# Optimization experiments

Hardware: AMD Instinct MI355X
Metric: run time of the kernel (lower is better)

## Reference

```python
import jax, jax.numpy as jnp
import numpy as np

# ---- static configuration (mirrors init_kwargs) ----
B, V, C, NH, HD = 1, 6, 256, 8, 32     # batch, views, embed, heads, head_dim
Z, L, P = 4, 4, 2                       # z-ref points, fmap levels, ref points
BEV_H, BEV_W = 80, 80
Q = BEV_H * BEV_W
IMG_H, IMG_W = 480, 800
LEVEL_SHAPES = [(60, 100), (30, 50), (15, 25), (8, 13)]
S = sum(h * w for h, w in LEVEL_SHAPES)
RES = 0.512
OFFSET_SCALE = 1.0
FF = 512


def layer_norm(x, g, b):
    m = jnp.mean(x, -1, keepdims=True)
    v = jnp.var(x, -1, keepdims=True)
    return (x - m) / jnp.sqrt(v + 1e-5) * g + b


def _bev_grid():
    xs = (jnp.arange(BEV_W) + 0.5) / BEV_W
    ys = (jnp.arange(BEV_H) + 0.5) / BEV_H
    gy, gx = jnp.meshgrid(ys, xs, indexing='ij')
    ref = jnp.stack([gx.reshape(-1), gy.reshape(-1)], -1)        # (Q,2) normalized xy
    world = (ref - 0.5) * jnp.array([BEV_W * RES, BEV_H * RES])  # (Q,2) ego-frame meters
    return ref, world


def deform_sample(value, H, W, loc):
    """Bilinear sampling. value: (N, H*W, NH, HD); loc: (N, Qn, NH, PP, 2) in [0,1].
    Returns (N, Qn, NH, PP, HD); out-of-bounds samples contribute zero."""
    v = jnp.moveaxis(value, 2, 1)                                # (N, NH, HW, HD)
    x = loc[..., 0] * W - 0.5
    y = loc[..., 1] * H - 0.5
    x0 = jnp.floor(x); y0 = jnp.floor(y)
    lx, ly = x - x0, y - y0
    x0 = x0.astype(jnp.int32); y0 = y0.astype(jnp.int32)
    gather = jax.vmap(jax.vmap(lambda vt, it: vt[it]))           # over (N, NH)
    def corner(xi, yi, w):
        ok = ((xi >= 0) & (xi < W) & (yi >= 0) & (yi < H)).astype(value.dtype)
        idx = jnp.clip(yi, 0, H - 1) * W + jnp.clip(xi, 0, W - 1)
        g = gather(v, jnp.moveaxis(idx, 2, 1))                   # (N,NH,Qn,PP,HD)
        return jnp.moveaxis(g, 1, 2) * (w * ok)[..., None]
    return (corner(x0, y0, (1 - lx) * (1 - ly)) + corner(x0 + 1, y0, lx * (1 - ly))
            + corner(x0, y0 + 1, (1 - lx) * ly) + corner(x0 + 1, y0 + 1, lx * ly))


def _forward(bev_queries, bev_histories, multiscale_fmaps, transition_matrices, z_refs,
             cam_proj_matrices, Wv_t, Woff_t, boff_t, Ww_t, bw_t, Wo_t, bo_t, ln1_g, ln1_b,
             Wv_s, Woff_s, boff_s, Ww_s, bw_s, Wo_s, bo_s, ln2_g, ln2_b,
             W1, b1, W2, b2, ln3_g, ln3_b):
    ref, world = _bev_grid()
    q = bev_queries
    # ---------- temporal self-attention (deformable over current + warped history) ----------
    vcur = (q @ Wv_t).reshape(B, Q, NH, HD)
    vhist = (bev_histories @ Wv_t).reshape(B, Q, NH, HD)
    off_t = (q @ Woff_t + boff_t).reshape(B, Q, NH, 2, P, 2) * OFFSET_SCALE
    w_t = jax.nn.softmax((q @ Ww_t + bw_t).reshape(B, Q, NH, 2 * P), -1).reshape(B, Q, NH, 2, P)
    ext = jnp.array([BEV_W * RES, BEV_H * RES], jnp.float32)
    wh = jnp.concatenate([world, jnp.ones((Q, 1), jnp.float32)], -1)     # (Q,3)
    warped = jnp.einsum('bij,qj->bqi', transition_matrices, wh)          # (B,Q,3)
    ref_hist = warped[..., :2] / warped[..., 2:3] / ext + 0.5            # (B,Q,2)
    norm_bev = jnp.array([BEV_W, BEV_H], jnp.float32)
    loc_c = ref[None, :, None, None, :] + off_t[:, :, :, 0] / norm_bev
    loc_h = ref_hist[:, :, None, None, :] + off_t[:, :, :, 1] / norm_bev
    s_c = deform_sample(vcur, BEV_H, BEV_W, loc_c)                       # (B,Q,NH,P,HD)
    s_h = deform_sample(vhist, BEV_H, BEV_W, loc_h)
    out_t = (jnp.einsum('bqhp,bqhpd->bqhd', w_t[:, :, :, 0], s_c)
             + jnp.einsum('bqhp,bqhpd->bqhd', w_t[:, :, :, 1], s_h))
    out1 = out_t.reshape(B, Q, C) @ Wo_t + bo_t
    out2 = layer_norm(out1 + q, ln1_g, ln1_b)
    # ---------- spatial cross-attention (multi-view multi-scale deformable) ----------
    val = (multiscale_fmaps @ Wv_s).reshape(B * V, S, NH, HD)
    pts = jnp.concatenate([
        jnp.broadcast_to(world[:, None, :], (Q, Z, 2)),
        jnp.broadcast_to(z_refs[None, :, None], (Q, Z, 1)),
        jnp.ones((Q, Z, 1), jnp.float32)], -1)                           # (Q,Z,4) homogeneous
    uvd = jnp.einsum('vij,qzj->vqzi', cam_proj_matrices, pts)            # (V,Q,Z,3)
    d = uvd[..., 2]
    un = uvd[..., 0] / jnp.maximum(d, 1e-5) / IMG_W
    vn = uvd[..., 1] / jnp.maximum(d, 1e-5) / IMG_H
    valid = ((d > 1e-5) & (un >= 0) & (un <= 1) & (vn >= 0) & (vn <= 1)).astype(q.dtype)
    refuv = jnp.stack([un, vn], -1)                                      # (V,Q,Z,2)
    off_s = (out2 @ Woff_s + boff_s).reshape(B, Q, NH, Z, L, P, 2) * OFFSET_SCALE
    w_s = jax.nn.softmax((out2 @ Ww_s + bw_s).reshape(B, Q, NH, Z * L * P), -1)
    w_s = w_s.reshape(B, Q, NH, Z, L, P)
    acc = jnp.zeros((B, Q, NH, HD), q.dtype)
    start = 0
    for l, (Hl, Wl) in enumerate(LEVEL_SHAPES):
        vl = val[:, start:start + Hl * Wl]
        start += Hl * Wl
        loc = (refuv[None, :, :, None, :, None, :]
               + off_s[:, None, :, :, :, l] / jnp.array([Wl, Hl], jnp.float32))
        loc = jnp.broadcast_to(loc, (B, V, Q, NH, Z, P, 2)).reshape(B * V, Q, NH, Z * P, 2)
        samp = deform_sample(vl, Hl, Wl, loc).reshape(B, V, Q, NH, Z, P, HD)
        wl = w_s[:, None, :, :, :, l] * valid[None, :, :, None, :, None]
        acc = acc + jnp.einsum('bvqhzp,bvqhzpd->bqhd', wl, samp)
    count = jnp.maximum(valid.sum((0, 2)), 1.0)                          # (Q,) hit count
    out3 = (acc / count[None, :, None, None]).reshape(B, Q, C) @ Wo_s + bo_s
    out4 = layer_norm(out3 + out2, ln2_g, ln2_b)
    # ---------- feed-forward ----------
    out5 = jax.nn.relu(out4 @ W1 + b1) @ W2 + b2
    return layer_norm(out5 + out4, ln3_g, ln3_b)


def setup_inputs() -> dict:
    key = jax.random.key(0)
    ks = iter(jax.random.split(key, 40))
    def rn(shape, s=1.0):
        return jax.random.normal(next(ks), shape, jnp.float32) * s
    sc = 1.0 / float(np.sqrt(C))
    inp = {}
    inp['bev_queries'] = rn((B, Q, C), 0.1)
    inp['bev_histories'] = rn((B, Q, C), 0.1)
    inp['multiscale_fmaps'] = rn((B, V, S, C), 0.1)
    th = 0.02
    T = np.array([[np.cos(th), -np.sin(th), 0.5],
                  [np.sin(th), np.cos(th), 0.1],
                  [0.0, 0.0, 1.0]], np.float32)
    inp['transition_matrices'] = jnp.tile(jnp.asarray(T)[None], (B, 1, 1))
    inp['z_refs'] = jnp.linspace(-5.0, 3.0, Z).astype(jnp.float32)
    K = np.array([[400.0, 0.0, IMG_W / 2], [0.0, 400.0, IMG_H / 2], [0.0, 0.0, 1.0]], np.float32)
    Ps = []
    for vi in range(V):
        a = 2 * np.pi * vi / V
        Rt = np.zeros((3, 4), np.float32)
        Rt[0, :3] = [-np.sin(a), np.cos(a), 0.0]   # camera right
        Rt[1, :3] = [0.0, 0.0, -1.0]               # camera down
        Rt[2, :3] = [np.cos(a), np.sin(a), 0.0]    # camera forward
        Ps.append(K @ Rt)
    inp['cam_proj_matrices'] = jnp.asarray(np.stack(Ps))
    # temporal self-attention params
    inp['Wv_t'] = rn((C, C), sc)
    inp['Woff_t'] = rn((C, NH * 2 * P * 2), sc * 0.1)
    inp['boff_t'] = jnp.zeros((NH * 2 * P * 2,), jnp.float32)
    inp['Ww_t'] = rn((C, NH * 2 * P), sc)
    inp['bw_t'] = jnp.zeros((NH * 2 * P,), jnp.float32)
    inp['Wo_t'] = rn((C, C), sc)
    inp['bo_t'] = jnp.zeros((C,), jnp.float32)
    inp['ln1_g'] = jnp.ones((C,), jnp.float32)
    inp['ln1_b'] = jnp.zeros((C,), jnp.float32)
    # spatial cross-attention params
    inp['Wv_s'] = rn((C, C), sc)
    inp['Woff_s'] = rn((C, NH * Z * L * P * 2), sc * 0.1)
    inp['boff_s'] = jnp.zeros((NH * Z * L * P * 2,), jnp.float32)
    inp['Ww_s'] = rn((C, NH * Z * L * P), sc)
    inp['bw_s'] = jnp.zeros((NH * Z * L * P,), jnp.float32)
    inp['Wo_s'] = rn((C, C), sc)
    inp['bo_s'] = jnp.zeros((C,), jnp.float32)
    inp['ln2_g'] = jnp.ones((C,), jnp.float32)
    inp['ln2_b'] = jnp.zeros((C,), jnp.float32)
    # FFN params
    inp['W1'] = rn((C, FF), sc)
    inp['b1'] = jnp.zeros((FF,), jnp.float32)
    inp['W2'] = rn((FF, C), 1.0 / float(np.sqrt(FF)))
    inp['b2'] = jnp.zeros((C,), jnp.float32)
    inp['ln3_g'] = jnp.ones((C,), jnp.float32)
    inp['ln3_b'] = jnp.zeros((C,), jnp.float32)
    # static shape descriptors (treated as compile-time constants)
    inp['bev_spatial_shape'] = np.array([[BEV_H, BEV_W]], np.int64)
    inp['multiscale_fmap_shapes'] = np.array(LEVEL_SHAPES, np.int64)
    inp['img_spatial_shape'] = np.array([[IMG_H, IMG_W]], np.int64)
    return inp


def reference(bev_queries, bev_histories, multiscale_fmaps, transition_matrices, z_refs,
              cam_proj_matrices, Wv_t, Woff_t, boff_t, Ww_t, bw_t, Wo_t, bo_t, ln1_g, ln1_b,
              Wv_s, Woff_s, boff_s, Ww_s, bw_s, Wo_s, bo_s, ln2_g, ln2_b,
              W1, b1, W2, b2, ln3_g, ln3_b,
              bev_spatial_shape, multiscale_fmap_shapes, img_spatial_shape):
    return _forward(bev_queries, bev_histories, multiscale_fmaps, transition_matrices, z_refs,
                    cam_proj_matrices, Wv_t, Woff_t, boff_t, Ww_t, bw_t, Wo_t, bo_t, ln1_g, ln1_b,
                    Wv_s, Woff_s, boff_s, Ww_s, bw_s, Wo_s, bo_s, ln2_g, ln2_b,
                    W1, b1, W2, b2, ln3_g, ln3_b)
```

## Files before the change

kernel.cpp:

```cpp
#include <hip/hip_runtime.h>
#include <hip/hip_bf16.h>
#include <hip/hip_fp16.h>

typedef unsigned short u16;
typedef unsigned int u32;
typedef __attribute__((ext_vector_type(8))) _Float16 f16x8;
typedef __attribute__((ext_vector_type(4))) float f32x4;

#define Q_N  6400
#define S_N  7979
#define BEV  80

__device__ __forceinline__ float f16tof(u16 u) {
    __half h; *(u16*)&h = u; return __half2float(h);
}
__device__ __forceinline__ u16 ftof16(float f) {
    __half h = __float2half(f); return *(u16*)&h;
}

template <int AIN, int RELU, int OUTMODE, int SM4, int SM32>
__device__ __forceinline__ void gemm_body(
    const void* __restrict__ A, const u16* __restrict__ WT,
    const float* __restrict__ bias, const float* __restrict__ bias2,
    void* __restrict__ Cout, int M, int N, int K, int bx, int by,
    u16* Ah, u16* Wh)
{
    const int tid  = threadIdx.x;
    const int lane = tid & 63;
    const int wave = tid >> 6;
    const int wm = (wave >> 1) * 32, wn = (wave & 1) * 64;
    const int m0 = by * 64, n0 = bx * 128;
    const int arow = tid >> 2, ak = (tid & 3) * 8;
    const int wrow = tid >> 1, wk = (tid & 1) * 16;
    const int fr = lane & 15, g = lane >> 4;

    f32x4 acc[8];
    #pragma unroll
    for (int i = 0; i < 8; ++i) acc[i] = (f32x4)(0.f);

    for (int k0 = 0; k0 < K; k0 += 32) {
        {
            const bool okr = (m0 + arow) < M;
            u16* dh = &Ah[arow * 40 + ak];
            if (AIN == 0) {
                const float* ap = (const float*)A + (size_t)(m0 + arow) * K + k0 + ak;
                float4 v0 = okr ? *(const float4*)(ap)     : make_float4(0.f, 0.f, 0.f, 0.f);
                float4 v1 = okr ? *(const float4*)(ap + 4) : make_float4(0.f, 0.f, 0.f, 0.f);
                u16 hb[8];
                hb[0] = ftof16(v0.x); hb[1] = ftof16(v0.y);
                hb[2] = ftof16(v0.z); hb[3] = ftof16(v0.w);
                hb[4] = ftof16(v1.x); hb[5] = ftof16(v1.y);
                hb[6] = ftof16(v1.z); hb[7] = ftof16(v1.w);
                *(ushort4*)(dh)     = *(ushort4*)&hb[0];
                *(ushort4*)(dh + 4) = *(ushort4*)&hb[4];
            } else {
                const u16* ap = (const u16*)A + (size_t)(m0 + arow) * K + k0 + ak;
                uint4 u = okr ? *(const uint4*)ap : make_uint4(0, 0, 0, 0);
                *(uint4*)dh = u;
            }
        }
        {
            const size_t wo = (size_t)(n0 + wrow) * K + k0 + wk;
            *(uint4*)&Wh[wrow * 40 + wk]     = *(const uint4*)(WT + wo);
            *(uint4*)&Wh[wrow * 40 + wk + 8] = *(const uint4*)(WT + wo + 8);
        }
        __syncthreads();
        f16x8 fah[2], fwh[4];
        #pragma unroll
        for (int i = 0; i < 2; ++i)
            fah[i] = *(const f16x8*)&Ah[(wm + i * 16 + fr) * 40 + g * 8];
        #pragma unroll
        for (int j = 0; j < 4; ++j)
            fwh[j] = *(const f16x8*)&Wh[(wn + j * 16 + fr) * 40 + g * 8];
        #pragma unroll
        for (int i = 0; i < 2; ++i)
            #pragma unroll
            for (int j = 0; j < 4; ++j)
                acc[i * 4 + j] = __builtin_amdgcn_mfma_f32_16x16x32_f16(fah[i], fwh[j], acc[i * 4 + j], 0, 0, 0);
        __syncthreads();
    }
    const int g4r = g * 4;
    float bv[4];
    #pragma unroll
    for (int j = 0; j < 4; ++j) {
        int col = n0 + wn + j * 16 + fr;
        if (bias2) bv[j] = (col < 512) ? bias[col] : bias2[col - 512];
        else       bv[j] = bias ? bias[col] : 0.f;
    }
    const bool do_sm4  = SM4 && (wn == 64);
    #pragma unroll
    for (int i = 0; i < 2; ++i) {
        #pragma unroll
        for (int r = 0; r < 4; ++r) {
            const int row = m0 + wm + i * 16 + g4r + r;
            float v0 = acc[i * 4 + 0][r] + bv[0];
            float v1 = acc[i * 4 + 1][r] + bv[1];
            float v2 = acc[i * 4 + 2][r] + bv[2];
            float v3 = acc[i * 4 + 3][r] + bv[3];
            if (RELU) {
                v0 = fmaxf(v0, 0.f); v1 = fmaxf(v1, 0.f);
                v2 = fmaxf(v2, 0.f); v3 = fmaxf(v3, 0.f);
            }
            if (SM4 && do_sm4) {
                float m0q = fmaxf(v0, __shfl_xor(v0, 1));
                m0q = fmaxf(m0q, __shfl_xor(m0q, 2));
                float e0 = __expf(v0 - m0q);
                float s0 = e0 + __shfl_xor(e0, 1);
                s0 += __shfl_xor(s0, 2);
                v0 = e0 / s0;
                float m1q = fmaxf(v1, __shfl_xor(v1, 1));
                m1q = fmaxf(m1q, __shfl_xor(m1q, 2));
                float e1 = __expf(v1 - m1q);
                float s1 = e1 + __shfl_xor(e1, 1);
                s1 += __shfl_xor(s1, 2);
                v1 = e1 / s1;
                v2 = 0.f; v3 = 0.f;
            }
            if (row < M) {
                const int colb = n0 + wn + fr;
                if (OUTMODE == 1) {
                    u16* cp = (u16*)Cout + (size_t)row * N;
                    cp[colb]      = ftof16(v0);
                    cp[colb + 16] = ftof16(v1);
                    cp[colb + 32] = ftof16(v2);
                    cp[colb + 48] = ftof16(v3);
                } else {
                    float* cp = (float*)Cout + (size_t)row * N;
                    cp[colb]      = v0;
                    cp[colb + 16] = v1;
                    cp[colb + 32] = v2;
                    cp[colb + 48] = v3;
                }
            }
        }
    }
}

__global__ __launch_bounds__(256) void fused3_k(
    const float* __restrict__ fmaps, const float* __restrict__ q, const float* __restrict__ hist,
    const u16* __restrict__ Wv_s_h, const u16* __restrict__ Wv_t_h,
    const u16* __restrict__ Wc_h, const float* __restrict__ bc,
    u16* __restrict__ val_f16, u16* __restrict__ vcur, u16* __restrict__ vhist,
    float* __restrict__ owt)
{
    __shared__ u16 Ah[64 * 40], Wh[128 * 40];
    const int b = blockIdx.x;
    if (b < 1498) {
        gemm_body<0, 0, 1, 0, 0>(fmaps, Wv_s_h, nullptr, nullptr, val_f16,
                                 47874, 256, 256, b & 1, b >> 1, Ah, Wh);
    } else if (b < 1698) {
        int l = b - 1498;
        gemm_body<0, 0, 1, 0, 0>(q, Wv_t_h, nullptr, nullptr, vcur,
                                 6400, 256, 256, l & 1, l >> 1, Ah, Wh);
    } else if (b < 1898) {
        int l = b - 1698;
        gemm_body<0, 0, 1, 0, 0>(hist, Wv_t_h, nullptr, nullptr, vhist,
                                 6400, 256, 256, l & 1, l >> 1, Ah, Wh);
    } else {
        int l = b - 1898;
        gemm_body<0, 0, 0, 1, 0>(q, Wc_h, bc, nullptr, owt,
                                 6400, 128, 256, 0, l, Ah, Wh);
    }
}

template <int AIN, int RELU, int OUTMODE, int SM4, int SM32>
__global__ __launch_bounds__(256, 2) void sgemm_k(
    const void* __restrict__ A, const u16* __restrict__ WT,
    const float* __restrict__ bias, const float* __restrict__ bias2,
    void* __restrict__ Cout, int M, int N, int K)
{
    __shared__ u16 Ah[8][1288];
    __shared__ u16 Wh[8][2568];
    const int tid  = threadIdx.x;
    const int lane = tid & 63;
    const int wave = tid >> 6;
    const int wm = (wave >> 1) * 16, wn = (wave & 1) * 32;
    const int m0 = blockIdx.y * 32, n0 = blockIdx.x * 64;
    const int fr = lane & 15, g = lane >> 4;

    const int ar  = tid >> 3, cch = tid & 7;
    const int wrow = tid >> 2, wc4 = tid & 3;

    f32x4 acc[2] = {(f32x4)(0.f), (f32x4)(0.f)};

    for (int k0 = 0; k0 < K; k0 += 256) {
        if (k0) __syncthreads();
        {
            const bool okr = (m0 + ar) < M;
            u16 hb[32];
            if (AIN == 0) {
                const float* ap = (const float*)A + (size_t)(m0 + ar) * K + k0 + cch * 32;
                #pragma unroll
                for (int i = 0; i < 8; ++i) {
                    float4 v = okr ? *(const float4*)(ap + i * 4) : make_float4(0.f, 0.f, 0.f, 0.f);
                    hb[i * 4 + 0] = ftof16(v.x); hb[i * 4 + 1] = ftof16(v.y);
                    hb[i * 4 + 2] = ftof16(v.z); hb[i * 4 + 3] = ftof16(v.w);
                }
            } else {
                const u16* ap = (const u16*)A + (size_t)(m0 + ar) * K + k0 + cch * 32;
                #pragma unroll
                for (int i = 0; i < 4; ++i)
                    *(uint4*)&hb[i * 8] = okr ? *(const uint4*)(ap + i * 8) : make_uint4(0, 0, 0, 0);
            }
            u16* dst = &Ah[cch][ar * 40];
            #pragma unroll
            for (int i = 0; i < 8; ++i)
                *(ushort4*)(dst + i * 4) = *(ushort4*)&hb[i * 4];
        }
        {
            const size_t wo = (size_t)(n0 + wrow) * K + k0 + wc4 * 64;
            #pragma unroll
            for (int half = 0; half < 2; ++half) {
                u16* dst = &Wh[wc4 * 2 + half][wrow * 40];
                const u16* src = WT + wo + half * 32;
                #pragma unroll
                for (int i = 0; i < 4; ++i)
                    *(uint4*)(dst + i * 8) = *(const uint4*)(src + i * 8);
            }
        }
        __syncthreads();
        #pragma unroll
        for (int c = 0; c < 8; ++c) {
            f16x8 fa  = *(const f16x8*)&Ah[c][(wm + fr) * 40 + g * 8];
            f16x8 fw0 = *(const f16x8*)&Wh[c][(wn + fr) * 40 + g * 8];
            f16x8 fw1 = *(const f16x8*)&Wh[c][(wn + 16 + fr) * 40 + g * 8];
            acc[0] = __builtin_amdgcn_mfma_f32_16x16x32_f16(fa, fw0, acc[0], 0, 0, 0);
            acc[1] = __builtin_amdgcn_mfma_f32_16x16x32_f16(fa, fw1, acc[1], 0, 0, 0);
        }
    }
    const int g4r = g * 4;
    const int c0g = n0 + wn + fr, c1g = c0g + 16;
    float bv0, bv1;
    if (bias2) {
        bv0 = (c0g < 512) ? bias[c0g] : bias2[c0g - 512];
        bv1 = (c1g < 512) ? bias[c1g] : bias2[c1g - 512];
    } else {
        bv0 = bias ? bias[c0g] : 0.f;
        bv1 = bias ? bias[c1g] : 0.f;
    }
    const bool do_sm32 = SM32 && ((n0 + wn) >= 512);
    const bool do_sm4  = SM4 && ((n0 + wn) == 64);
    const bool zr4     = SM4 && ((n0 + wn) == 96);
    #pragma unroll
    for (int r = 0; r < 4; ++r) {
        const int row = m0 + wm + g4r + r;
        float v0 = acc[0][r] + bv0;
        float v1 = acc[1][r] + bv1;
        if (RELU) { v0 = fmaxf(v0, 0.f); v1 = fmaxf(v1, 0.f); }
        if (SM4) {
            if (do_sm4) {
                float m0q = fmaxf(v0, __shfl_xor(v0, 1));
                m0q = fmaxf(m0q, __shfl_xor(m0q, 2));
                float e0 = __expf(v0 - m0q);
                float s0 = e0 + __shfl_xor(e0, 1);
                s0 += __shfl_xor(s0, 2);
                v0 = e0 / s0;
                float m1q = fmaxf(v1, __shfl_xor(v1, 1));
                m1q = fmaxf(m1q, __shfl_xor(m1q, 2));
                float e1 = __expf(v1 - m1q);
                float s1 = e1 + __shfl_xor(e1, 1);
                s1 += __shfl_xor(s1, 2);
                v1 = e1 / s1;
            }
            if (zr4) { v0 = 0.f; v1 = 0.f; }
        }
        if (SM32 && do_sm32) {
            float ma = fmaxf(v0, v1);
            ma = fmaxf(ma, __shfl_xor(ma, 1));
            ma = fmaxf(ma, __shfl_xor(ma, 2));
            ma = fmaxf(ma, __shfl_xor(ma, 4));
            ma = fmaxf(ma, __shfl_xor(ma, 8));
            float e0 = __expf(v0 - ma), e1 = __expf(v1 - ma);
            float sa = e0 + e1;
            sa += __shfl_xor(sa, 1);
            sa += __shfl_xor(sa, 2);
            sa += __shfl_xor(sa, 4);
            sa += __shfl_xor(sa, 8);
            float ia = 1.f / sa;
            v0 = e0 * ia; v1 = e1 * ia;
        }
        if (row < M) {
            if (OUTMODE == 1) {
                u16* cp = (u16*)Cout + (size_t)row * N;
                cp[c0g] = ftof16(v0);
                cp[c1g] = ftof16(v1);
            } else {
                float* cp = (float*)Cout + (size_t)row * N;
                cp[c0g] = v0;
                cp[c1g] = v1;
            }
        }
    }
}

__global__ __launch_bounds__(256) void wprep_k(
    const float* __restrict__ w0, const float* __restrict__ w1, const float* __restrict__ w2,
    const float* __restrict__ w3, const float* __restrict__ w4, const float* __restrict__ w5,
    const float* __restrict__ w6, const float* __restrict__ w7, u16* __restrict__ base,
    const float* __restrict__ Woff_t, const float* __restrict__ Ww_t,
    const float* __restrict__ boff_t, const float* __restrict__ bw_t,
    float* __restrict__ bc)
{
    const int b = blockIdx.x, tid = threadIdx.x;
    if (b == 184) {
        if (tid < 128) bc[tid] = (tid < 64) ? boff_t[tid] : (tid < 96 ? bw_t[tid - 64] : 0.f);
        return;
    }
    const int cum[10]  = {0, 16, 32, 48, 80, 96, 112, 144, 176, 184};
    const int Ks[9]    = {256, 256, 256, 256, 256, 256, 256, 512, 256};
    const int Ns[9]    = {256, 256, 256, 512, 256, 256, 512, 256, 128};
    const int hoff[9]  = {0, 65536, 131072, 196608, 327680, 393216, 458752, 589824, 720896};
    int seg = 0;
    #pragma unroll
    for (int s = 1; s < 9; ++s) if (b >= cum[s]) seg = s;
    const int K = Ks[seg], N = Ns[seg];
    const int t = b - cum[seg];
    const int ntn = N / 64;
    const int k0 = (t / ntn) * 64, n0 = (t % ntn) * 64;
    __shared__ float tile[64][65];
    const int rr = tid >> 2, cc = (tid & 3) * 16;
    if (seg < 8) {
        const float* W = seg == 0 ? w0 : seg == 1 ? w1 : seg == 2 ? w2 : seg == 3 ? w3 :
                         seg == 4 ? w4 : seg == 5 ? w5 : seg == 6 ? w6 : w7;
        #pragma unroll
        for (int c = 0; c < 4; ++c) {
            float4 v = *(const float4*)(W + (size_t)(k0 + rr) * N + n0 + cc + c * 4);
            tile[rr][cc + c * 4 + 0] = v.x;
            tile[rr][cc + c * 4 + 1] = v.y;
            tile[rr][cc + c * 4 + 2] = v.z;
            tile[rr][cc + c * 4 + 3] = v.w;
        }
    } else {
        #pragma unroll
        for (int i = 0; i < 16; ++i) {
            int n = n0 + cc + i, k = k0 + rr;
            float v = (n < 64) ? Woff_t[k * 64 + n] : (n < 96 ? Ww_t[k * 32 + n - 64] : 0.f);
            tile[rr][cc + i] = v;
        }
    }
    __syncthreads();
    const int nr = tid >> 2, kc = (tid & 3) * 16;
    u16 hb[16];
    #pragma unroll
    for (int i = 0; i < 16; ++i) hb[i] = ftof16(tile[kc + i][nr]);
    u16* hp = base + hoff[seg] + (size_t)(n0 + nr) * K + k0 + kc;
    *(ushort4*)(hp + 0)  = *(ushort4*)&hb[0];
    *(ushort4*)(hp + 4)  = *(ushort4*)&hb[4];
    *(ushort4*)(hp + 8)  = *(ushort4*)&hb[8];
    *(ushort4*)(hp + 12) = *(ushort4*)&hb[12];
}

__global__ __launch_bounds__(256) void ln_k(
    const float* __restrict__ x, const float* __restrict__ res,
    const float* __restrict__ g, const float* __restrict__ b,
    float* __restrict__ out)
{
    const int row = blockIdx.x, t = threadIdx.x;
    const size_t idx = (size_t)row * 256 + t;
    float v = x[idx] + res[idx];
    float s = v, ss = v * v;
    #pragma unroll
    for (int o = 32; o > 0; o >>= 1) {
        s += __shfl_down(s, o);
        ss += __shfl_down(ss, o);
    }
    __shared__ float red[8];
    __shared__ float mv[2];
    const int wv = t >> 6, ln = t & 63;
    if (ln == 0) { red[wv] = s; red[4 + wv] = ss; }
    __syncthreads();
    if (t == 0) {
        float S = red[0] + red[1] + red[2] + red[3];
        float SS = red[4] + red[5] + red[6] + red[7];
        float mean = S * (1.f / 256.f);
        float var = SS * (1.f / 256.f) - mean * mean;
        mv[0] = mean;
        mv[1] = rsqrtf(var + 1e-5f);
    }
    __syncthreads();
    out[idx] = (v - mv[0]) * mv[1] * g[t] + b[t];
}

__device__ __forceinline__ float4 bilin4h(const u16* __restrict__ v, int H, int W,
                                          float x, float y, int chb)
{
    float xf = floorf(x), yf = floorf(y);
    int x0 = (int)xf, y0 = (int)yf;
    int x1 = x0 + 1, y1 = y0 + 1;
    float fx = x - xf, fy = y - yf;
    float w00 = (1.f - fx) * (1.f - fy), w10 = fx * (1.f - fy);
    float w01 = (1.f - fx) * fy,         w11 = fx * fy;
    bool xi0 = (x0 >= 0) && (x0 < W);
    bool xi1 = (x1 >= 0) && (x1 < W);
    bool yi0 = (y0 >= 0) && (y0 < H);
    bool yi1 = (y1 >= 0) && (y1 < H);
    float4 r = make_float4(0.f, 0.f, 0.f, 0.f);
    #define CORNER(xi, yi, xx, yy, ww)                                           \
        if ((yi) && (xi)) {                                                      \
            uint2 u = *(const uint2*)(v + ((size_t)(yy) * W + (xx)) * 256 + chb);\
            float2 f0 = __half22float2(*(const __half2*)&u.x);                   \
            float2 f1 = __half22float2(*(const __half2*)&u.y);                   \
            r.x += (ww) * f0.x; r.y += (ww) * f0.y;                              \
            r.z += (ww) * f1.x; r.w += (ww) * f1.y;                              \
        }
    CORNER(xi0, yi0, x0, y0, w00)
    CORNER(xi1, yi0, x1, y0, w10)
    CORNER(xi0, yi1, x0, y1, w01)
    CORNER(xi1, yi1, x1, y1, w11)
    #undef CORNER
    return r;
}

__global__ __launch_bounds__(256) void temporal_k(
    const u16* __restrict__ vcur, const u16* __restrict__ vhist,
    const float* __restrict__ ow,
    const float* __restrict__ Tm, float* __restrict__ outt)
{
    const int b = blockIdx.x;
    const int q = (b & 7) * 800 + (b >> 3);
    const int tid = threadIdx.x;
    const int c4 = tid & 63, rep = tid >> 6;
    const int br = rep >> 1, p = rep & 1;
    const int h = c4 >> 3;
    const int chb = h * 32 + (c4 & 7) * 4;
    const int jx = q % BEV, iy = q / BEV;
    const float refx = (jx + 0.5f) / 80.f;
    const float refy = (iy + 0.5f) / 80.f;
    const float wx = (refx - 0.5f) * 40.96f;
    const float wy = (refy - 0.5f) * 40.96f;
    float bx, by;
    const u16* v;
    if (br == 0) { v = vcur; bx = refx; by = refy; }
    else {
        float h0 = Tm[0] * wx + Tm[1] * wy + Tm[2];
        float h1 = Tm[3] * wx + Tm[4] * wy + Tm[5];
        float h2 = Tm[6] * wx + Tm[7] * wy + Tm[8];
        v = vhist;
        bx = h0 / h2 / 40.96f + 0.5f;
        by = h1 / h2 / 40.96f + 0.5f;
    }
    const float* owq = ow + (size_t)q * 128;
    int ob = h * 8 + br * 4 + p * 2;
// ... 50 lines not shown
        const u16* owq = ow + (size_t)q * 768;
        #pragma unroll
        for (int rep = 0; rep < 2; ++rep) {
            int flat = tid + rep * 256;
            int hh = flat >> 6, rem = flat & 63;
            int zz = rem >> 4, ll = (rem >> 2) & 3, pp = (rem >> 1) & 1, xy = rem & 1;
            int dst = (zz * 8 + ll * 2 + pp) * 8 + hh;
            float v = f16tof(owq[flat]);
            if (xy) s_oy[dst] = v; else s_ox[dst] = v;
        }
        int hh = tid >> 5, rem = tid & 31;
        s_wt[rem * 8 + hh] = f16tof(owq[512 + tid]);
    }
    __syncthreads();
    if (tid == 0) {
        int n = 0; float c = 0.f;
        for (int vz = 0; vz < 24; ++vz) {
            if (s_ok[vz] != 0.f) { s_list[n++] = vz; c += 1.f; }
        }
        s_n = n; s_cnt = fmaxf(c, 1.f);
    }
    __syncthreads();
    const int n4 = s_n * 4;
    float a0 = 0.f, a1 = 0.f, a2 = 0.f, a3 = 0.f, a4 = 0.f, a5 = 0.f, a6 = 0.f, a7 = 0.f;
    for (int w = slot; w < n4; w += 8) {
        const int it = w >> 2, l = w & 3;
        const int vz = s_list[it];
        const int v = vz >> 2, z = vz & 3;
        const float un = s_un[vz], vn = s_vn[vz];
        const int Hl  = (l == 0) ? 60  : (l == 1) ? 30   : (l == 2) ? 15   : 8;
        const int Wl  = (l == 0) ? 100 : (l == 1) ? 50   : (l == 2) ? 25   : 13;
        const int LSo = (l == 0) ? 0   : (l == 1) ? 6000 : (l == 2) ? 7500 : 7875;
        const u16* lv = val + ((size_t)v * S_N + LSo) * 256 + chb;
        const float unl = un * Wl - 0.5f, vnl = vn * Hl - 0.5f;
        const int Ws = Wl * 256;
        #pragma unroll
        for (int p = 0; p < 2; ++p) {
            const int idx = (z * 8 + l * 2 + p) * 8 + h;
            float x = unl + s_ox[idx];
            float y = vnl + s_oy[idx];
            float wgt = s_wt[idx];
            float xf = floorf(x), yf = floorf(y);
            int x0 = (int)xf, y0 = (int)yf;
            float fx = x - xf, fy = y - yf;
            bool xi0 = (x0 >= 0) & (x0 < Wl);
            bool xi1 = (x0 >= -1) & (x0 < Wl - 1);
            bool yi0 = (y0 >= 0) & (y0 < Hl);
            bool yi1 = (y0 >= -1) & (y0 < Hl - 1);
            int xc0 = min(max(x0, 0), Wl - 1);
            int xc1 = min(max(x0 + 1, 0), Wl - 1);
            int yc0 = min(max(y0, 0), Hl - 1);
            int yc1 = min(max(y0 + 1, 0), Hl - 1);
            float m00 = (xi0 & yi0) ? wgt : 0.f;
            float m10 = (xi1 & yi0) ? wgt : 0.f;
            float m01 = (xi0 & yi1) ? wgt : 0.f;
            float m11 = (xi1 & yi1) ? wgt : 0.f;
            __half2 w00 = __float2half2_rn((1.f - fx) * (1.f - fy) * m00);
            __half2 w10 = __float2half2_rn(fx * (1.f - fy) * m10);
            __half2 w01 = __float2half2_rn((1.f - fx) * fy * m01);
            __half2 w11 = __float2half2_rn(fx * fy * m11);
            const u16* r0p = lv + (size_t)yc0 * Ws;
            const u16* r1p = lv + (size_t)yc1 * Ws;
            uint4 u00 = *(const uint4*)(r0p + (size_t)xc0 * 256);
            uint4 u10 = *(const uint4*)(r0p + (size_t)xc1 * 256);
            uint4 u01 = *(const uint4*)(r1p + (size_t)xc0 * 256);
            uint4 u11 = *(const uint4*)(r1p + (size_t)xc1 * 256);
            __half2 h0 = __float2half2_rn(0.f), h1 = h0, h2 = h0, h3 = h0;
            {
                const __half2* hp = (const __half2*)&u00;
                h0 = __hfma2(w00, hp[0], h0); h1 = __hfma2(w00, hp[1], h1);
                h2 = __hfma2(w00, hp[2], h2); h3 = __hfma2(w00, hp[3], h3);
            }
            {
                const __half2* hp = (const __half2*)&u10;
                h0 = __hfma2(w10, hp[0], h0); h1 = __hfma2(w10, hp[1], h1);
                h2 = __hfma2(w10, hp[2], h2); h3 = __hfma2(w10, hp[3], h3);
            }
            {
                const __half2* hp = (const __half2*)&u01;
                h0 = __hfma2(w01, hp[0], h0); h1 = __hfma2(w01, hp[1], h1);
                h2 = __hfma2(w01, hp[2], h2); h3 = __hfma2(w01, hp[3], h3);
            }
            {
                const __half2* hp = (const __half2*)&u11;
                h0 = __hfma2(w11, hp[0], h0); h1 = __hfma2(w11, hp[1], h1);
                h2 = __hfma2(w11, hp[2], h2); h3 = __hfma2(w11, hp[3], h3);
            }
            float2 f0 = __half22float2(h0), f1 = __half22float2(h1);
            float2 f2 = __half22float2(h2), f3 = __half22float2(h3);
            a0 += f0.x; a1 += f0.y; a2 += f1.x; a3 += f1.y;
            a4 += f2.x; a5 += f2.y; a6 += f3.x; a7 += f3.y;
        }
    }
    *(float4*)&s_part[slot][chb]     = make_float4(a0, a1, a2, a3);
    *(float4*)&s_part[slot][chb + 4] = make_float4(a4, a5, a6, a7);
    __syncthreads();
    float sum = 0.f;
    #pragma unroll
    for (int k = 0; k < 8; ++k) sum += s_part[k][tid];
    out[(size_t)q * 256 + tid] = sum / s_cnt;
}

extern "C" void kernel_launch(void* const* d_in, const int* in_sizes, int n_in,
                              void* d_out, int out_size, void* d_ws, size_t ws_size,
                              hipStream_t stream) {
    (void)in_sizes; (void)n_in; (void)out_size; (void)ws_size;
    const float* q      = (const float*)d_in[0];
    const float* hist   = (const float*)d_in[1];
    const float* fmaps  = (const float*)d_in[2];
    const float* Tm     = (const float*)d_in[3];
    const float* zrefs  = (const float*)d_in[4];
    const float* cam    = (const float*)d_in[5];
    const float* Woff_t = (const float*)d_in[7];
    const float* boff_t = (const float*)d_in[8];
    const float* Ww_t   = (const float*)d_in[9];
    const float* bw_t   = (const float*)d_in[10];
    const float* bo_t   = (const float*)d_in[12];
    const float* ln1g   = (const float*)d_in[13];
    const float* ln1b   = (const float*)d_in[14];
    const float* boff_s = (const float*)d_in[17];
    const float* bw_s   = (const float*)d_in[19];
    const float* bo_s   = (const float*)d_in[21];
    const float* ln2g   = (const float*)d_in[22];
    const float* ln2b   = (const float*)d_in[23];
    const float* b1     = (const float*)d_in[25];
    const float* b2     = (const float*)d_in[27];
    const float* ln3g   = (const float*)d_in[28];
    const float* ln3b   = (const float*)d_in[29];

    float* ws    = (float*)d_ws;
    float* r0    = ws;
    float* r1    = ws + 1638400;
    float* owt   = ws + 3276800;
    float* r4    = ws + 4096000;
    u16*  r5u    = (u16*)(ws + 5734400);
    float* of4   = ws + 8192000;
    u16*  valbuf = (u16*)(ws + 9830400);
    u16*  vcur   = (u16*)(ws + 15958272);
    u16*  vhist  = (u16*)(ws + 16777472);
    u16*  wtab   = (u16*)(ws + 17596672);
    float* bc    = ws + 18350336;

    u16* hidden = valbuf;
    u16* Wv_t_h = wtab + 0;
    u16* Wo_t_h = wtab + 65536;
    u16* Wv_s_h = wtab + 131072;
    u16* Comb_h = wtab + 196608;
    u16* Wo_s_h = wtab + 393216;
    u16* W1_h   = wtab + 458752;
    u16* W2_h   = wtab + 589824;
    u16* Wc_h   = wtab + 720896;

    dim3 blk(256);
    auto gs = [](int M, int N) { return dim3((unsigned)(N / 64), (unsigned)((M + 31) / 32)); };

    wprep_k<<<dim3(185), blk, 0, stream>>>(
        (const float*)d_in[6], (const float*)d_in[11], (const float*)d_in[15],
        (const float*)d_in[16], (const float*)d_in[18], (const float*)d_in[20],
        (const float*)d_in[24], (const float*)d_in[26], wtab,
        Woff_t, Ww_t, boff_t, bw_t, bc);
    fused3_k<<<dim3(1998), blk, 0, stream>>>(
        fmaps, q, hist, Wv_s_h, Wv_t_h, Wc_h, bc,
        valbuf, vcur, vhist, owt);
    temporal_k<<<dim3(6400), blk, 0, stream>>>(vcur, vhist, owt, Tm, r4);
    sgemm_k<0,0,0,0,0><<<gs(6400, 256), blk, 0, stream>>>(
        r4, Wo_t_h, bo_t, nullptr, r0, 6400, 256, 256);
    ln_k<<<dim3(6400), blk, 0, stream>>>(r0, q, ln1g, ln1b, r1);
    sgemm_k<0,0,1,0,1><<<gs(6400, 768), blk, 0, stream>>>(
        r1, Comb_h, boff_s, bw_s, r5u, 6400, 768, 256);
    spatial_k<<<dim3(6400), blk, 0, stream>>>(valbuf, r5u, cam, zrefs, r0);
    sgemm_k<0,0,0,0,0><<<gs(6400, 256), blk, 0, stream>>>(
        r0, Wo_s_h, bo_s, nullptr, r4, 6400, 256, 256);
    ln_k<<<dim3(6400), blk, 0, stream>>>(r4, r1, ln2g, ln2b, of4);
    sgemm_k<0,1,1,0,0><<<gs(6400, 512), blk, 0, stream>>>(
        of4, W1_h, b1, nullptr, hidden, 6400, 512, 256);
    sgemm_k<1,0,0,0,0><<<gs(6400, 256), blk, 0, stream>>>(
        hidden, W2_h, b2, nullptr, r0, 6400, 256, 512);
    ln_k<<<dim3(6400), blk, 0, stream>>>(r0, of4, ln3g, ln3b, (float*)d_out);
}
```

Measured before the change: 360.4 us.

## Fuse residual LayerNorm into GEMM A-load and retile GEMMs to 64-row blocks

Replaces the sgemm kernel with a 64x64-tile GEMM that keeps the full 256-wide A strip in shared memory and streams weight K-slices through a double buffer. Two standalone LayerNorm launches are removed: the following GEMM adds the residual, normalizes each row while loading A, and has the blockIdx.x==0 blocks write the normalized rows out for later residual use. This cuts launches and the global round trip for the LN outputs. In exchange every N-block recomputes the LN, and a __syncthreads now runs after each 32-wide K step.

After: 368.1 us. 2.1% more time.

```diff
diff --git a/kernel.cpp b/kernel.cpp
--- a/kernel.cpp
+++ b/kernel.cpp
@@ -163,69 +163,112 @@
     }
 }
 
-template <int AIN, int RELU, int OUTMODE, int SM4, int SM32>
-__global__ __launch_bounds__(256, 2) void sgemm_k(
-    const void* __restrict__ A, const u16* __restrict__ WT,
-    const float* __restrict__ bias, const float* __restrict__ bias2,
+template <int AIN, int RELU, int OUTMODE, int SM32, int LNA>
+__global__ __launch_bounds__(256) void mgemm2_k(
+    const void* __restrict__ A, const float* __restrict__ res,
+    const float* __restrict__ lng, const float* __restrict__ lnb,
+    float* __restrict__ aux,
+    const u16* __restrict__ WT, const float* __restrict__ bias, const float* __restrict__ bias2,
     void* __restrict__ Cout, int M, int N, int K)
 {
-    __shared__ u16 Ah[8][1288];
-    __shared__ u16 Wh[8][2568];
+    __shared__ u16 As[64 * 264];
+    __shared__ u16 Wsh[2][64 * 40];
     const int tid  = threadIdx.x;
     const int lane = tid & 63;
     const int wave = tid >> 6;
-    const int wm = (wave >> 1) * 16, wn = (wave & 1) * 32;
-    const int m0 = blockIdx.y * 32, n0 = blockIdx.x * 64;
+    const int wm = (wave >> 1) * 32, wn = (wave & 1) * 32;
+    const int m0 = blockIdx.y * 64, n0 = blockIdx.x * 64;
     const int fr = lane & 15, g = lane >> 4;
-
-    const int ar  = tid >> 3, cch = tid & 7;
-    const int wrow = tid >> 2, wc4 = tid & 3;
-
-    f32x4 acc[2] = {(f32x4)(0.f), (f32x4)(0.f)};
-
-    for (int k0 = 0; k0 < K; k0 += 256) {
-        if (k0) __syncthreads();
+    const int ar = tid >> 2, aq = tid & 3;
+    const int NSTEP = K >> 5;
+
+    f32x4 acc[4];
+    #pragma unroll
+    for (int i = 0; i < 4; ++i) acc[i] = (f32x4)(0.f);
+
+    for (int kh = 0; kh < K; kh += 256) {
         {
             const bool okr = (m0 + ar) < M;
-            u16 hb[32];
             if (AIN == 0) {
-                const float* ap = (const float*)A + (size_t)(m0 + ar) * K + k0 + cch * 32;
-                #pragma unroll
-                for (int i = 0; i < 8; ++i) {
-                    float4 v = okr ? *(const float4*)(ap + i * 4) : make_float4(0.f, 0.f, 0.f, 0.f);
-                    hb[i * 4 + 0] = ftof16(v.x); hb[i * 4 + 1] = ftof16(v.y);
-                    hb[i * 4 + 2] = ftof16(v.z); hb[i * 4 + 3] = ftof16(v.w);
+                const float* ap = (const float*)A + (size_t)(m0 + ar) * K + kh;
+                if (LNA) {
+                    float4 vals[16];
+                    float s = 0.f, ss = 0.f;
+                    const float* rp = res + (size_t)(m0 + ar) * 256;
+                    #pragma unroll
+                    for (int j = 0; j < 16; ++j) {
+                        const int k = aq * 4 + j * 16;
+                        float4 x = okr ? *(const float4*)(ap + k) : make_float4(0.f, 0.f, 0.f, 0.f);
+                        float4 rr = okr ? *(const float4*)(rp + k) : make_float4(0.f, 0.f, 0.f, 0.f);
+                        x.x += rr.x; x.y += rr.y; x.z += rr.z; x.w += rr.w;
+                        vals[j] = x;
+                        s += x.x + x.y + x.z + x.w;
+                        ss += x.x * x.x + x.y * x.y + x.z * x.z + x.w * x.w;
+                    }
+                    s  += __shfl_xor(s, 1);  s  += __shfl_xor(s, 2);
+                    ss += __shfl_xor(ss, 1); ss += __shfl_xor(ss, 2);
+                    const float mean = s * (1.f / 256.f);
+                    const float rstd = rsqrtf(ss * (1.f / 256.f) - mean * mean + 1e-5f);
+                    const bool wa = (blockIdx.x == 0) && okr;
+                    #pragma unroll
+                    for (int j = 0; j < 16; ++j) {
+                        const int k = aq * 4 + j * 16;
+                        float4 g4 = *(const float4*)(lng + k);
+                        float4 b4 = *(const float4*)(lnb + k);
+                        float4 v = vals[j];
+                        v.x = (v.x - mean) * rstd * g4.x + b4.x;
+                        v.y = (v.y - mean) * rstd * g4.y + b4.y;
+                        v.z = (v.z - mean) * rstd * g4.z + b4.z;
+                        v.w = (v.w - mean) * rstd * g4.w + b4.w;
+                        if (wa) *(float4*)(aux + (size_t)(m0 + ar) * 256 + k) = v;
+                        u16 hb[4];
+                        hb[0] = ftof16(v.x); hb[1] = ftof16(v.y);
+                        hb[2] = ftof16(v.z); hb[3] = ftof16(v.w);
+                        *(ushort4*)&As[ar * 264 + k] = *(ushort4*)&hb[0];
+                    }
+                } else {
+                    #pragma unroll
+                    for (int j = 0; j < 16; ++j) {
+                        const int k = aq * 4 + j * 16;
+                        float4 x = okr ? *(const float4*)(ap + k) : make_float4(0.f, 0.f, 0.f, 0.f);
+                        u16 hb[4];
+                        hb[0] = ftof16(x.x); hb[1] = ftof16(x.y);
+                        hb[2] = ftof16(x.z); hb[3] = ftof16(x.w);
+                        *(ushort4*)&As[ar * 264 + k] = *(ushort4*)&hb[0];
+                    }
                 }
             } else {
-                const u16* ap = (const u16*)A + (size_t)(m0 + ar) * K + k0 + cch * 32;
+                const u16* ap = (const u16*)A + (size_t)(m0 + ar) * K + kh;
                 #pragma unroll
-                for (int i = 0; i < 4; ++i)
-                    *(uint4*)&hb[i * 8] = okr ? *(const uint4*)(ap + i * 8) : make_uint4(0, 0, 0, 0);
-            }
-            u16* dst = &Ah[cch][ar * 40];
-            #pragma unroll
-            for (int i = 0; i < 8; ++i)
-                *(ushort4*)(dst + i * 4) = *(ushort4*)&hb[i * 4];
-        }
-        {
-            const size_t wo = (size_t)(n0 + wrow) * K + k0 + wc4 * 64;
-            #pragma unroll
-            for (int half = 0; half < 2; ++half) {
-                u16* dst = &Wh[wc4 * 2 + half][wrow * 40];
-                const u16* src = WT + wo + half * 32;
-                #pragma unroll
-                for (int i = 0; i < 4; ++i)
-                    *(uint4*)(dst + i * 8) = *(const uint4*)(src + i * 8);
-            }
+                for (int j = 0; j < 8; ++j) {
+                    const int k = aq * 8 + j * 32;
+                    uint4 u = okr ? *(const uint4*)(ap + k) : make_uint4(0, 0, 0, 0);
+                    *(uint4*)&As[ar * 264 + k] = u;
+                }
+            }
+        }
+        if (kh == 0) {
+            *(uint4*)&Wsh[0][ar * 40 + aq * 8] =
+                *(const uint4*)(WT + (size_t)(n0 + ar) * K + aq * 8);
         }
         __syncthreads();
         #pragma unroll
-        for (int c = 0; c < 8; ++c) {
-            f16x8 fa  = *(const f16x8*)&Ah[c][(wm + fr) * 40 + g * 8];
-            f16x8 fw0 = *(const f16x8*)&Wh[c][(wn + fr) * 40 + g * 8];
-            f16x8 fw1 = *(const f16x8*)&Wh[c][(wn + 16 + fr) * 40 + g * 8];
-            acc[0] = __builtin_amdgcn_mfma_f32_16x16x32_f16(fa, fw0, acc[0], 0, 0, 0);
-            acc[1] = __builtin_amdgcn_mfma_f32_16x16x32_f16(fa, fw1, acc[1], 0, 0, 0);
+        for (int s = 0; s < 8; ++s) {
+            const int gstep = (kh >> 5) + s;
+            const int nxt = gstep + 1;
+            if (nxt < NSTEP) {
+                *(uint4*)&Wsh[nxt & 1][ar * 40 + aq * 8] =
+                    *(const uint4*)(WT + (size_t)(n0 + ar) * K + nxt * 32 + aq * 8);
+            }
+            f16x8 fa0 = *(const f16x8*)&As[(wm + fr) * 264 + s * 32 + g * 8];
+            f16x8 fa1 = *(const f16x8*)&As[(wm + 16 + fr) * 264 + s * 32 + g * 8];
+            f16x8 fw0 = *(const f16x8*)&Wsh[s & 1][(wn + fr) * 40 + g * 8];
+            f16x8 fw1 = *(const f16x8*)&Wsh[s & 1][(wn + 16 + fr) * 40 + g * 8];
+            acc[0] = __builtin_amdgcn_mfma_f32_16x16x32_f16(fa0, fw0, acc[0], 0, 0, 0);
+            acc[1] = __builtin_amdgcn_mfma_f32_16x16x32_f16(fa0, fw1, acc[1], 0, 0, 0);
+            acc[2] = __builtin_amdgcn_mfma_f32_16x16x32_f16(fa1, fw0, acc[2], 0, 0, 0);
+            acc[3] = __builtin_amdgcn_mfma_f32_16x16x32_f16(fa1, fw1, acc[3], 0, 0, 0);
+            __syncthreads();
         }
     }
     const int g4r = g * 4;
@@ -239,55 +282,39 @@
         bv1 = bias ? bias[c1g] : 0.f;
     }
     const bool do_sm32 = SM32 && ((n0 + wn) >= 512);
-    const bool do_sm4  = SM4 && ((n0 + wn) == 64);
-    const bool zr4     = SM4 && ((n0 + wn) == 96);
-    #pragma unroll
-    for (int r = 0; r < 4; ++r) {
-        const int row = m0 + wm + g4r + r;
-        float v0 = acc[0][r] + bv0;
-        float v1 = acc[1][r] + bv1;
-        if (RELU) { v0 = fmaxf(v0, 0.f); v1 = fmaxf(v1, 0.f); }
-        if (SM4) {
-            if (do_sm4) {
-                float m0q = fmaxf(v0, __shfl_xor(v0, 1));
-                m0q = fmaxf(m0q, __shfl_xor(m0q, 2));
-                float e0 = __expf(v0 - m0q);
-                float s0 = e0 + __shfl_xor(e0, 1);
-                s0 += __shfl_xor(s0, 2);
-                v0 = e0 / s0;
-                float m1q = fmaxf(v1, __shfl_xor(v1, 1));
-                m1q = fmaxf(m1q, __shfl_xor(m1q, 2));
-                float e1 = __expf(v1 - m1q);
-                float s1 = e1 + __shfl_xor(e1, 1);
-                s1 += __shfl_xor(s1, 2);
-                v1 = e1 / s1;
-            }
-            if (zr4) { v0 = 0.f; v1 = 0.f; }
-        }
-        if (SM32 && do_sm32) {
-            float ma = fmaxf(v0, v1);
-            ma = fmaxf(ma, __shfl_xor(ma, 1));
-            ma = fmaxf(ma, __shfl_xor(ma, 2));
-            ma = fmaxf(ma, __shfl_xor(ma, 4));
-            ma = fmaxf(ma, __shfl_xor(ma, 8));
-            float e0 = __expf(v0 - ma), e1 = __expf(v1 - ma);
-            float sa = e0 + e1;
-            sa += __shfl_xor(sa, 1);
-            sa += __shfl_xor(sa, 2);
-            sa += __shfl_xor(sa, 4);
-            sa += __shfl_xor(sa, 8);
-            float ia = 1.f / sa;
-            v0 = e0 * ia; v1 = e1 * ia;
-        }
-        if (row < M) {
-            if (OUTMODE == 1) {
-                u16* cp = (u16*)Cout + (size_t)row * N;
-                cp[c0g] = ftof16(v0);
-                cp[c1g] = ftof16(v1);
-            } else {
-                float* cp = (float*)Cout + (size_t)row * N;
-                cp[c0g] = v0;
-                cp[c1g] = v1;
+    #pragma unroll
+    for (int i = 0; i < 2; ++i) {
+        #pragma unroll
+        for (int r = 0; r < 4; ++r) {
+            const int row = m0 + wm + i * 16 + g4r + r;
+            float v0 = acc[i * 2 + 0][r] + bv0;
+            float v1 = acc[i * 2 + 1][r] + bv1;
+            if (RELU) { v0 = fmaxf(v0, 0.f); v1 = fmaxf(v1, 0.f); }
+            if (SM32 && do_sm32) {
+                float ma = fmaxf(v0, v1);
+                ma = fmaxf(ma, __shfl_xor(ma, 1));
+                ma = fmaxf(ma, __shfl_xor(ma, 2));
+                ma = fmaxf(ma, __shfl_xor(ma, 4));
+                ma = fmaxf(ma, __shfl_xor(ma, 8));
+                float e0 = __expf(v0 - ma), e1 = __expf(v1 - ma);
+                float sa = e0 + e1;
+                sa += __shfl_xor(sa, 1);
+                sa += __shfl_xor(sa, 2);
+                sa += __shfl_xor(sa, 4);
+                sa += __shfl_xor(sa, 8);
+                float ia = 1.f / sa;
+                v0 = e0 * ia; v1 = e1 * ia;
+            }
+            if (row < M) {
+                if (OUTMODE == 1) {
+                    u16* cp = (u16*)Cout + (size_t)row * N;
+                    cp[c0g] = ftof16(v0);
+                    cp[c1g] = ftof16(v1);
+                } else {
+                    float* cp = (float*)Cout + (size_t)row * N;
+                    cp[c0g] = v0;
+                    cp[c1g] = v1;
+                }
             }
         }
     }
@@ -644,7 +671,7 @@
     u16* Wc_h   = wtab + 720896;
 
     dim3 blk(256);
-    auto gs = [](int M, int N) { return dim3((unsigned)(N / 64), (unsigned)((M + 31) / 32)); };
+    auto g2 = [](int M, int N) { return dim3((unsigned)(N / 64), (unsigned)((M + 63) / 64)); };
 
     wprep_k<<<dim3(185), blk, 0, stream>>>(
         (const float*)d_in[6], (const float*)d_in[11], (const float*)d_in[15],
@@ -655,18 +682,21 @@
         fmaps, q, hist, Wv_s_h, Wv_t_h, Wc_h, bc,
         valbuf, vcur, vhist, owt);
     temporal_k<<<dim3(6400), blk, 0, stream>>>(vcur, vhist, owt, Tm, r4);
-    sgemm_k<0,0,0,0,0><<<gs(6400, 256), blk, 0, stream>>>(
-        r4, Wo_t_h, bo_t, nullptr, r0, 6400, 256, 256);
-    ln_k<<<dim3(6400), blk, 0, stream>>>(r0, q, ln1g, ln1b, r1);
-    sgemm_k<0,0,1,0,1><<<gs(6400, 768), blk, 0, stream>>>(
-        r1, Comb_h, boff_s, bw_s, r5u, 6400, 768, 256);
+    mgemm2_k<0,0,0,0,0><<<g2(6400, 256), blk, 0, stream>>>(
+        r4, nullptr, nullptr, nullptr, nullptr,
+        Wo_t_h, bo_t, nullptr, r0, 6400, 256, 256);
+    mgemm2_k<0,0,1,1,1><<<g2(6400, 768), blk, 0, stream>>>(
+        r0, q, ln1g, ln1b, r1,
+        Comb_h, boff_s, bw_s, r5u, 6400, 768, 256);
     spatial_k<<<dim3(6400), blk, 0, stream>>>(valbuf, r5u, cam, zrefs, r0);
-    sgemm_k<0,0,0,0,0><<<gs(6400, 256), blk, 0, stream>>>(
-        r0, Wo_s_h, bo_s, nullptr, r4, 6400, 256, 256);
-    ln_k<<<dim3(6400), blk, 0, stream>>>(r4, r1, ln2g, ln2b, of4);
-    sgemm_k<0,1,1,0,0><<<gs(6400, 512), blk, 0, stream>>>(
-        of4, W1_h, b1, nullptr, hidden, 6400, 512, 256);
-    sgemm_k<1,0,0,0,0><<<gs(6400, 256), blk, 0, stream>>>(
-        hidden, W2_h, b2, nullptr, r0, 6400, 256, 512);
+    mgemm2_k<0,0,0,0,0><<<g2(6400, 256), blk, 0, stream>>>(
+        r0, nullptr, nullptr, nullptr, nullptr,
+        Wo_s_h, bo_s, nullptr, r4, 6400, 256, 256);
+    mgemm2_k<0,1,1,0,1><<<g2(6400, 512), blk, 0, stream>>>(
+        r4, r1, ln2g, ln2b, of4,
+        W1_h, b1, nullptr, hidden, 6400, 512, 256);
+    mgemm2_k<1,0,0,0,0><<<g2(6400, 256), blk, 0, stream>>>(
+        hidden, nullptr, nullptr, nullptr, nullptr,
+        W2_h, b2, nullptr, r0, 6400, 256, 512);
     ln_k<<<dim3(6400), blk, 0, stream>>>(r0, of4, ln3g, ln3b, (float*)d_out);
 }
```

## Double-buffer GEMM K-loop with register prefetch and swizzled block order

Applied to the files above, without the earlier changes.

Replaces the standalone GEMM kernel's staging of the full 256-wide K slice into large shared memory with a 32-wide K step that is double-buffered. The next slice is prefetched into registers while the MFMAs run on the current one. Shared memory per block drops sharply, launch bounds move to 4 blocks per CU, and workgroup IDs are remapped in groups of 8 to change cache locality. The cost is one barrier per 32-wide K step instead of per 256, plus removal of the row-bound check and the unused SM4 path. That is safe here because M is a multiple of 32.

Result: faster. 304.4 us (-15.6%).

```diff
diff --git a/kernel.cpp b/kernel.cpp
--- a/kernel.cpp
+++ b/kernel.cpp
@@ -163,72 +163,75 @@
     }
 }
 
-template <int AIN, int RELU, int OUTMODE, int SM4, int SM32>
-__global__ __launch_bounds__(256, 2) void sgemm_k(
+template <int AIN, int RELU, int OUTMODE, int SM32>
+__global__ __launch_bounds__(256, 4) void cgemm_k(
     const void* __restrict__ A, const u16* __restrict__ WT,
     const float* __restrict__ bias, const float* __restrict__ bias2,
     void* __restrict__ Cout, int M, int N, int K)
 {
-    __shared__ u16 Ah[8][1288];
-    __shared__ u16 Wh[8][2568];
+    __shared__ u16 As[2][32 * 40];
+    __shared__ u16 Wsh[2][64 * 40];
     const int tid  = threadIdx.x;
     const int lane = tid & 63;
     const int wave = tid >> 6;
     const int wm = (wave >> 1) * 16, wn = (wave & 1) * 32;
-    const int m0 = blockIdx.y * 32, n0 = blockIdx.x * 64;
     const int fr = lane & 15, g = lane >> 4;
-
-    const int ar  = tid >> 3, cch = tid & 7;
-    const int wrow = tid >> 2, wc4 = tid & 3;
+    const int nx = gridDim.x;
+    const int nwg = nx * gridDim.y;
+    const int o = blockIdx.y * nx + blockIdx.x;
+    const int flat = (o & 7) * (nwg >> 3) + (o >> 3);
+    const int bx = flat % nx, by = flat / nx;
+    const int m0 = by * 32, n0 = bx * 64;
+    const int ar = tid >> 3, ak = (tid & 7) * 4;
+    const int wr = tid >> 2, wk = (tid & 3) * 8;
+    const int NS = K >> 5;
 
     f32x4 acc[2] = {(f32x4)(0.f), (f32x4)(0.f)};
 
-    for (int k0 = 0; k0 < K; k0 += 256) {
-        if (k0) __syncthreads();
-        {
-            const bool okr = (m0 + ar) < M;
-            u16 hb[32];
+    const float* apf = (const float*)A + (size_t)(m0 + ar) * K + ak;
+    const u16*  aph  = (const u16*)A + (size_t)(m0 + ar) * K + ak;
+    const u16*  wp   = WT + (size_t)(n0 + wr) * K + wk;
+
+    if (AIN == 0) {
+        float4 v = *(const float4*)apf;
+        u16 hb[4];
+        hb[0] = ftof16(v.x); hb[1] = ftof16(v.y); hb[2] = ftof16(v.z); hb[3] = ftof16(v.w);
+        *(ushort4*)&As[0][ar * 40 + ak] = *(ushort4*)&hb[0];
+    } else {
+        *(uint2*)&As[0][ar * 40 + ak] = *(const uint2*)aph;
+    }
+    *(uint4*)&Wsh[0][wr * 40 + wk] = *(const uint4*)wp;
+    __syncthreads();
+
+    for (int s = 0; s < NS; ++s) {
+        float4 av; uint2 au; uint4 wv;
+        const bool pf = (s + 1) < NS;
+        if (pf) {
+            if (AIN == 0) av = *(const float4*)(apf + (s + 1) * 32);
+            else          au = *(const uint2*)(aph + (s + 1) * 32);
+            wv = *(const uint4*)(wp + (s + 1) * 32);
+        }
+        const int b = s & 1;
+        f16x8 fa  = *(const f16x8*)&As[b][(wm + fr) * 40 + g * 8];
+        f16x8 fw0 = *(const f16x8*)&Wsh[b][(wn + fr) * 40 + g * 8];
+        f16x8 fw1 = *(const f16x8*)&Wsh[b][(wn + 16 + fr) * 40 + g * 8];
+        acc[0] = __builtin_amdgcn_mfma_f32_16x16x32_f16(fa, fw0, acc[0], 0, 0, 0);
+        acc[1] = __builtin_amdgcn_mfma_f32_16x16x32_f16(fa, fw1, acc[1], 0, 0, 0);
+        if (pf) {
+            const int nb = b ^ 1;
             if (AIN == 0) {
-                const float* ap = (const float*)A + (size_t)(m0 + ar) * K + k0 + cch * 32;
-                #pragma unroll
-                for (int i = 0; i < 8; ++i) {
-                    float4 v = okr ? *(const float4*)(ap + i * 4) : make_float4(0.f, 0.f, 0.f, 0.f);
-                    hb[i * 4 + 0] = ftof16(v.x); hb[i * 4 + 1] = ftof16(v.y);
-                    hb[i * 4 + 2] = ftof16(v.z); hb[i * 4 + 3] = ftof16(v.w);
-                }
+                u16 hb[4];
+                hb[0] = ftof16(av.x); hb[1] = ftof16(av.y);
+                hb[2] = ftof16(av.z); hb[3] = ftof16(av.w);
+                *(ushort4*)&As[nb][ar * 40 + ak] = *(ushort4*)&hb[0];
             } else {
-                const u16* ap = (const u16*)A + (size_t)(m0 + ar) * K + k0 + cch * 32;
-                #pragma unroll
-                for (int i = 0; i < 4; ++i)
-                    *(uint4*)&hb[i * 8] = okr ? *(const uint4*)(ap + i * 8) : make_uint4(0, 0, 0, 0);
-            }
-            u16* dst = &Ah[cch][ar * 40];
-            #pragma unroll
-            for (int i = 0; i < 8; ++i)
-                *(ushort4*)(dst + i * 4) = *(ushort4*)&hb[i * 4];
-        }
-        {
-            const size_t wo = (size_t)(n0 + wrow) * K + k0 + wc4 * 64;
-            #pragma unroll
-            for (int half = 0; half < 2; ++half) {
-                u16* dst = &Wh[wc4 * 2 + half][wrow * 40];
-                const u16* src = WT + wo + half * 32;
-                #pragma unroll
-                for (int i = 0; i < 4; ++i)
-                    *(uint4*)(dst + i * 8) = *(const uint4*)(src + i * 8);
-            }
+                *(uint2*)&As[nb][ar * 40 + ak] = au;
+            }
+            *(uint4*)&Wsh[nb][wr * 40 + wk] = wv;
         }
         __syncthreads();
-        #pragma unroll
-        for (int c = 0; c < 8; ++c) {
-            f16x8 fa  = *(const f16x8*)&Ah[c][(wm + fr) * 40 + g * 8];
-            f16x8 fw0 = *(const f16x8*)&Wh[c][(wn + fr) * 40 + g * 8];
-            f16x8 fw1 = *(const f16x8*)&Wh[c][(wn + 16 + fr) * 40 + g * 8];
-            acc[0] = __builtin_amdgcn_mfma_f32_16x16x32_f16(fa, fw0, acc[0], 0, 0, 0);
-            acc[1] = __builtin_amdgcn_mfma_f32_16x16x32_f16(fa, fw1, acc[1], 0, 0, 0);
-        }
-    }
-    const int g4r = g * 4;
+    }
+
     const int c0g = n0 + wn + fr, c1g = c0g + 16;
     float bv0, bv1;
     if (bias2) {
@@ -239,31 +242,12 @@
         bv1 = bias ? bias[c1g] : 0.f;
     }
     const bool do_sm32 = SM32 && ((n0 + wn) >= 512);
-    const bool do_sm4  = SM4 && ((n0 + wn) == 64);
-    const bool zr4     = SM4 && ((n0 + wn) == 96);
     #pragma unroll
     for (int r = 0; r < 4; ++r) {
-        const int row = m0 + wm + g4r + r;
+        const int row = m0 + wm + g * 4 + r;
         float v0 = acc[0][r] + bv0;
         float v1 = acc[1][r] + bv1;
         if (RELU) { v0 = fmaxf(v0, 0.f); v1 = fmaxf(v1, 0.f); }
-        if (SM4) {
-            if (do_sm4) {
-                float m0q = fmaxf(v0, __shfl_xor(v0, 1));
-                m0q = fmaxf(m0q, __shfl_xor(m0q, 2));
-                float e0 = __expf(v0 - m0q);
-                float s0 = e0 + __shfl_xor(e0, 1);
-                s0 += __shfl_xor(s0, 2);
-                v0 = e0 / s0;
-                float m1q = fmaxf(v1, __shfl_xor(v1, 1));
-                m1q = fmaxf(m1q, __shfl_xor(m1q, 2));
-                float e1 = __expf(v1 - m1q);
-                float s1 = e1 + __shfl_xor(e1, 1);
-                s1 += __shfl_xor(s1, 2);
-                v1 = e1 / s1;
-            }
-            if (zr4) { v0 = 0.f; v1 = 0.f; }
-        }
         if (SM32 && do_sm32) {
             float ma = fmaxf(v0, v1);
             ma = fmaxf(ma, __shfl_xor(ma, 1));
@@ -644,7 +628,7 @@
     u16* Wc_h   = wtab + 720896;
 
     dim3 blk(256);
-    auto gs = [](int M, int N) { return dim3((unsigned)(N / 64), (unsigned)((M + 31) / 32)); };
+    auto gc = [](int M, int N) { return dim3((unsigned)(N / 64), (unsigned)((M + 31) / 32)); };
 
     wprep_k<<<dim3(185), blk, 0, stream>>>(
         (const float*)d_in[6], (const float*)d_in[11], (const float*)d_in[15],
@@ -655,18 +639,18 @@
         fmaps, q, hist, Wv_s_h, Wv_t_h, Wc_h, bc,
         valbuf, vcur, vhist, owt);
     temporal_k<<<dim3(6400), blk, 0, stream>>>(vcur, vhist, owt, Tm, r4);
-    sgemm_k<0,0,0,0,0><<<gs(6400, 256), blk, 0, stream>>>(
+    cgemm_k<0,0,0,0><<<gc(6400, 256), blk, 0, stream>>>(
         r4, Wo_t_h, bo_t, nullptr, r0, 6400, 256, 256);
     ln_k<<<dim3(6400), blk, 0, stream>>>(r0, q, ln1g, ln1b, r1);
-    sgemm_k<0,0,1,0,1><<<gs(6400, 768), blk, 0, stream>>>(
+    cgemm_k<0,0,1,1><<<gc(6400, 768), blk, 0, stream>>>(
         r1, Comb_h, boff_s, bw_s, r5u, 6400, 768, 256);
     spatial_k<<<dim3(6400), blk, 0, stream>>>(valbuf, r5u, cam, zrefs, r0);
-    sgemm_k<0,0,0,0,0><<<gs(6400, 256), blk, 0, stream>>>(
+    cgemm_k<0,0,0,0><<<gc(6400, 256), blk, 0, stream>>>(
         r0, Wo_s_h, bo_s, nullptr, r4, 6400, 256, 256);
     ln_k<<<dim3(6400), blk, 0, stream>>>(r4, r1, ln2g, ln2b, of4);
-    sgemm_k<0,1,1,0,0><<<gs(6400, 512), blk, 0, stream>>>(
+    cgemm_k<0,1,1,0><<<gc(6400, 512), blk, 0, stream>>>(
         of4, W1_h, b1, nullptr, hidden, 6400, 512, 256);
-    sgemm_k<1,0,0,0,0><<<gs(6400, 256), blk, 0, stream>>>(
+    cgemm_k<1,0,0,0><<<gc(6400, 256), blk, 0, stream>>>(
         hidden, W2_h, b2, nullptr, r0, 6400, 256, 512);
     ln_k<<<dim3(6400), blk, 0, stream>>>(r0, of4, ln3g, ln3b, (float*)d_out);
 }
```
